# Performance work log

Hardware: AMD Instinct MI355X
Metric: run time of the kernel (lower is better)

Reference implementation:

```python
import jax, jax.numpy as jnp
import numpy as np

B, T, D = 4, 2048, 768
H = 12
HD = D // H
WINDOW = 128

def setup_inputs() -> dict:
    key = jax.random.key(0)
    k1, k2, k3 = jax.random.split(key, 3)
    x = jax.random.normal(k1, (B, T, D), dtype=jnp.float32)
    Wqkv = jax.random.normal(k2, (D, 3 * D), dtype=jnp.float32) * 0.02
    Wout = jax.random.normal(k3, (D, D), dtype=jnp.float32) * 0.02
    return {"x": x, "Wqkv": Wqkv, "Wout": Wout}

def reference(x, Wqkv, Wout):
    Bx, Tx, Dx = x.shape
    qkv = x @ Wqkv                      # [B,T,3D]
    q, k, v = jnp.split(qkv, 3, axis=-1)
    def heads(t):
        return t.reshape(Bx, Tx, H, HD).transpose(0, 2, 1, 3)  # [B,H,T,hd]
    q, k, v = heads(q), heads(k), heads(v)
    scale = 1.0 / jnp.sqrt(jnp.float32(HD))
    scores = jnp.einsum('bhqd,bhkd->bhqk', q, k) * scale       # [B,H,T,T]
    pos = jnp.arange(Tx)
    dist = pos[None, :] - pos[:, None]                          # j - i
    blocked = (dist > 0) | (dist < -WINDOW)                     # causal band
    scores = jnp.where(blocked[None, None], -jnp.inf, scores)
    attn = jax.nn.softmax(scores, axis=-1)
    out = jnp.einsum('bhqk,bhkd->bhqd', attn, v)                # [B,H,T,hd]
    out = out.transpose(0, 2, 1, 3).reshape(Bx, Tx, Dx)
    return out @ Wout
```

## Files before the change

### kernel.cpp

```cpp
#include <hip/hip_runtime.h>
#include <hip/hip_bf16.h>
#include <stdint.h>

typedef unsigned short u16;
typedef __attribute__((ext_vector_type(8))) short short8;
typedef __attribute__((ext_vector_type(8))) __bf16 bf16x8;
typedef __attribute__((ext_vector_type(4))) float f32x4;

constexpr int Bc  = 4;
constexpr int Tc  = 2048;
constexpr int Dc  = 768;
constexpr int Hc  = 12;
constexpr int WINc = 128;

static __device__ __forceinline__ u16 f2bf(float f) {
  union { float f; uint32_t u; } v; v.f = f;
  uint32_t u = v.u;
  return (u16)((u + 0x7fffu + ((u >> 16) & 1u)) >> 16);
}

static __device__ __forceinline__ f32x4 mfma16x16x32(bf16x8 a, bf16x8 b, f32x4 c) {
  return __builtin_amdgcn_mfma_f32_16x16x32_bf16(a, b, c, 0, 0, 0);
}

#define GLOAD_LDS16(gsrc, ldst)                                                \
  __builtin_amdgcn_global_load_lds(                                            \
      (const __attribute__((address_space(1))) void*)(gsrc),                   \
      (__attribute__((address_space(3))) void*)(ldst), 16, 0, 0)

__global__ __launch_bounds__(256) void prep(const float* __restrict__ x,
                                            u16* __restrict__ xb,
                                            const float* __restrict__ Wqkv,
                                            u16* __restrict__ wqkvT,
                                            const float* __restrict__ Wout,
                                            u16* __restrict__ woutT) {
  __shared__ float tile[64][65];
  const int t = threadIdx.x;
  const int b = blockIdx.x;
  if (b < 6144) {
    const int i = b * 256 + t;
    const float4 f = ((const float4*)x)[i];
    union { u16 h[4]; uint2 u; } pk;
    pk.h[0] = f2bf(f.x); pk.h[1] = f2bf(f.y); pk.h[2] = f2bf(f.z); pk.h[3] = f2bf(f.w);
    ((uint2*)xb)[i] = pk.u;
    return;
  }
  const float* W; u16* WT; int C, bx, by;
  if (b < 6576) { W = Wqkv; WT = wqkvT; C = 2304; const int bb = b - 6144; bx = bb % 36; by = bb / 36; }
  else          { W = Wout; WT = woutT; C = 768;  const int bb = b - 6576; bx = bb % 12; by = bb / 12; }
  const int R = 768;
  const int c0 = bx * 64, r0 = by * 64;
#pragma unroll
  for (int i = 0; i < 16; ++i) {
    const int e = i * 256 + t;
    const int r = e >> 6, c = e & 63;
    tile[r][c] = W[(size_t)(r0 + r) * C + c0 + c];
  }
  __syncthreads();
#pragma unroll
  for (int i = 0; i < 16; ++i) {
    const int e = i * 256 + t;
    const int r = e >> 6, c = e & 63;
    WT[(size_t)(c0 + r) * R + r0 + c] = f2bf(tile[c][r]);
  }
}

template <int EPI>
__global__ __launch_bounds__(256) void gemm_bt(const u16* __restrict__ A,
                                               const u16* __restrict__ Bt,
                                               u16* __restrict__ q_ws,
                                               u16* __restrict__ k_ws,
                                               u16* __restrict__ v_ws,
                                               float* __restrict__ fout) {
  __shared__ u16 As[2][128][64];
  __shared__ u16 Bs[2][128][64];
  const int t  = threadIdx.x;
  const int w  = t >> 6, l = t & 63;
  const int lr = l & 15, lh = l >> 4;
  const int wm = w >> 1, wn = w & 1;
  const int m0 = blockIdx.y * 128, n0 = blockIdx.x * 128;

  f32x4 acc[4][4];
#pragma unroll
  for (int mi = 0; mi < 4; ++mi)
#pragma unroll
    for (int ni = 0; ni < 4; ++ni) acc[mi][ni] = f32x4{0.f, 0.f, 0.f, 0.f};

  const int srow = w * 8 + (l >> 3);
  const int scol = ((l & 7) ^ (l >> 3)) * 8;
  const u16* aP = A  + (size_t)(m0 + srow) * 768 + scol;
  const u16* bP = Bt + (size_t)(n0 + srow) * 768 + scol;

#define STAGE(kt, b)                                                           \
  {                                                                            \
    const int ko_ = (kt) * 64;                                                 \
    char* asB_ = (char*)As + (b) * 16384 + w * 1024;                           \
    char* bsB_ = (char*)Bs + (b) * 16384 + w * 1024;                           \
    _Pragma("unroll")                                                          \
    for (int j = 0; j < 4; ++j) {                                              \
      GLOAD_LDS16(aP + ko_ + j * (32 * 768), asB_ + j * 4096);                 \
      GLOAD_LDS16(bP + ko_ + j * (32 * 768), bsB_ + j * 4096);                 \
    }                                                                          \
  }

#define COMPUTE(b)                                                             \
  {                                                                            \
    _Pragma("unroll")                                                          \
    for (int kk = 0; kk < 2; ++kk) {                                           \
      const int cb = (kk * 64 + lh * 16) ^ ((lr & 7) << 4);                    \
      bf16x8 af[4], bfr[4];                                                    \
      _Pragma("unroll")                                                        \
      for (int mi = 0; mi < 4; ++mi)                                           \
        af[mi] = *(const bf16x8*)((const char*)As + (b) * 16384 +              \
                                  (wm * 64 + mi * 16 + lr) * 128 + cb);        \
      _Pragma("unroll")                                                        \
      for (int ni = 0; ni < 4; ++ni)                                           \
        bfr[ni] = *(const bf16x8*)((const char*)Bs + (b) * 16384 +             \
                                   (wn * 64 + ni * 16 + lr) * 128 + cb);       \
      _Pragma("unroll")                                                        \
      for (int mi = 0; mi < 4; ++mi)                                           \
        _Pragma("unroll")                                                      \
        for (int ni = 0; ni < 4; ++ni)                                         \
          acc[mi][ni] = mfma16x16x32(af[mi], bfr[ni], acc[mi][ni]);            \
    }                                                                          \
  }

  STAGE(0, 0);
  for (int kt = 0; kt < 11; ++kt) {
    const int b = kt & 1;
    STAGE(kt + 1, b ^ 1);
    asm volatile("s_waitcnt vmcnt(8)" ::: "memory");
    __builtin_amdgcn_sched_barrier(0);
    __builtin_amdgcn_s_barrier();
    COMPUTE(b);
    __builtin_amdgcn_s_barrier();
  }
  asm volatile("s_waitcnt vmcnt(0)" ::: "memory");
  __builtin_amdgcn_sched_barrier(0);
  __builtin_amdgcn_s_barrier();
  COMPUTE(1);

#undef STAGE
#undef COMPUTE

  if (EPI == 0) {
#pragma unroll
    for (int mi = 0; mi < 4; ++mi)
#pragma unroll
      for (int ni = 0; ni < 4; ++ni) {
        const int col   = n0 + wn * 64 + ni * 16 + lr;
        const int which = col / 768;
        const int rem   = col - which * 768;
        const int h     = rem >> 6, d = rem & 63;
        u16* dst = (which == 0) ? q_ws : ((which == 1) ? k_ws : v_ws);
        const float scl = (which == 0) ? 0.125f : 1.0f;
#pragma unroll
        for (int r = 0; r < 4; ++r) {
          const int m  = m0 + wm * 64 + mi * 16 + lh * 4 + r;
          const int bb = m >> 11, tt = m & 2047;
          dst[(((size_t)(bb * Hc + h) * Tc + tt) << 6) + d] = f2bf(acc[mi][ni][r] * scl);
        }
      }
  } else {
#pragma unroll
    for (int mi = 0; mi < 4; ++mi)
#pragma unroll
      for (int ni = 0; ni < 4; ++ni) {
        const int col = n0 + wn * 64 + ni * 16 + lr;
#pragma unroll
        for (int r = 0; r < 4; ++r) {
          const int m = m0 + wm * 64 + mi * 16 + lh * 4 + r;
          fout[(size_t)m * 768 + col] = acc[mi][ni][r];
        }
      }
  }
}

__global__ __launch_bounds__(256) void swa_attn(const u16* __restrict__ Q,
                                                const u16* __restrict__ Kk,
                                                const u16* __restrict__ V,
                                                u16* __restrict__ Out) {
  __shared__ u16 Ks[3][64][72];
  __shared__ u16 Vt[3][64][72];
  __shared__ u16 Ps[2][4][16][72];

  const int t  = threadIdx.x;
  const int w  = t >> 6, l = t & 63;
  const int lr = l & 15, lh = l >> 4;
  const int bh = blockIdx.y;
  const int q0 = blockIdx.x * 64;
  const size_t hb = (size_t)bh * Tc * 64;

  const int kb_lo = (q0 >= WINc) ? q0 - WINc : 0;
  const int nt    = ((q0 - kb_lo) >> 6) + 1;

  const u16* qrow = Q + hb + (size_t)(q0 + w * 16 + lr) * 64;
  const bf16x8 qa0 = *(const bf16x8*)(qrow + lh * 8);
  const bf16x8 qa1 = *(const bf16x8*)(qrow + 32 + lh * 8);

  const int row = t >> 2, c = (t & 3) * 16;
  short8 kreg[3][2], vreg[3][2];
#pragma unroll
  for (int ti = 0; ti < 3; ++ti) {
    if (ti < nt) {
      const int kb = kb_lo + ti * 64;
      const short8* ksrc = (const short8*)(Kk + hb + (size_t)(kb + row) * 64 + c);
      const short8* vsrc = (const short8*)(V  + hb + (size_t)(kb + row) * 64 + c);
      kreg[ti][0] = ksrc[0]; kreg[ti][1] = ksrc[1];
      vreg[ti][0] = vsrc[0]; vreg[ti][1] = vsrc[1];
    }
  }
#pragma unroll
  for (int ti = 0; ti < 3; ++ti) {
    if (ti < nt) {
      *(short8*)&Ks[ti][row][c]     = kreg[ti][0];
      *(short8*)&Ks[ti][row][c + 8] = kreg[ti][1];
      const int rsw = row ^ c;
#pragma unroll
      for (int j = 0; j < 8; ++j) {
        Vt[ti][c + j][rsw]     = (u16)vreg[ti][0][j];
        Vt[ti][c + 8 + j][rsw] = (u16)vreg[ti][1][j];
      }
    }
  }
  __syncthreads();

  const short8 ones_i = {(short)0x3F80, (short)0x3F80, (short)0x3F80, (short)0x3F80,
                         (short)0x3F80, (short)0x3F80, (short)0x3F80, (short)0x3F80};
  const bf16x8 onesv = *(const bf16x8*)&ones_i;

  f32x4 s[3][4];
#pragma unroll
  for (int ti = 0; ti < 3; ++ti) {
    if (ti < nt) {
#pragma unroll
      for (int sub = 0; sub < 4; ++sub) {
        const bf16x8 kb0 = *(const bf16x8*)&Ks[ti][sub * 16 + lr][lh * 8];
        const bf16x8 kb1 = *(const bf16x8*)&Ks[ti][sub * 16 + lr][32 + lh * 8];
        f32x4 z = f32x4{0.f, 0.f, 0.f, 0.f};
        z = mfma16x16x32(qa0, kb0, z);
        z = mfma16x16x32(qa1, kb1, z);
        s[ti][sub] = z;
      }
    }
  }

  const int qbase = q0 + w * 16 + lh * 4;
#pragma unroll
  for (int ti = 0; ti < 3; ++ti) {
    if (ti < nt) {
      const int kb = kb_lo + ti * 64;
#pragma unroll
      for (int sub = 0; sub < 4; ++sub) {
        const int kj = kb + sub * 16 + lr;
#pragma unroll
        for (int r = 0; r < 4; ++r) {
          const int qi = qbase + r;
          const bool ok = (kj <= qi) && (kj + WINc >= qi);
          s[ti][sub][r] = ok ? s[ti][sub][r] : -1e30f;
        }
      }
    }
  }

  float m_r[4];
#pragma unroll
  for (int r = 0; r < 4; ++r) m_r[r] = -1e30f;
#pragma unroll
  for (int ti = 0; ti < 3; ++ti)
    if (ti < nt)
#pragma unroll
      for (int sub = 0; sub < 4; ++sub)
#pragma unroll
        for (int r = 0; r < 4; ++r)
          m_r[r] = fmaxf(m_r[r], s[ti][sub][r]);
#pragma unroll
  for (int msk = 1; msk < 16; msk <<= 1)
#pragma unroll
    for (int r = 0; r < 4; ++r)
      m_r[r] = fmaxf(m_r[r], __shfl_xor(m_r[r], msk, 64));

#pragma unroll
  for (int ti = 0; ti < 3; ++ti)
    if (ti < nt)
#pragma unroll
      for (int sub = 0; sub < 4; ++sub)
#pragma unroll
        for (int r = 0; r < 4; ++r)
          s[ti][sub][r] = __expf(s[ti][sub][r] - m_r[r]);

  f32x4 lacc = f32x4{0.f, 0.f, 0.f, 0.f};
  f32x4 Oa[4];
#pragma unroll
  for (int n = 0; n < 4; ++n) Oa[n] = f32x4{0.f, 0.f, 0.f, 0.f};

#pragma unroll
  for (int ti = 0; ti < 3; ++ti) {
    if (ti < nt) {
      const int pb = ti & 1;
#pragma unroll
      for (int sub = 0; sub < 4; ++sub)
#pragma unroll
        for (int r = 0; r < 4; ++r)
          Ps[pb][w][lh * 4 + r][sub * 16 + lr] = f2bf(s[ti][sub][r]);

#pragma unroll
      for (int ks = 0; ks < 2; ++ks) {
        const bf16x8 pa = *(const bf16x8*)&Ps[pb][w][lr][ks * 32 + lh * 8];
        lacc = mfma16x16x32(pa, onesv, lacc);
#pragma unroll
        for (int n = 0; n < 4; ++n) {
          const bf16x8 vb =
              *(const bf16x8*)&Vt[ti][n * 16 + lr][(ks * 32 + lh * 8) ^ (n * 16)];
          Oa[n] = mfma16x16x32(pa, vb, Oa[n]);
        }
      }
    }
  }

  const int bb = bh / Hc, h = bh - bb * Hc;
#pragma unroll
  for (int r = 0; r < 4; ++r) {
    const float inv = 1.f / lacc[r];
    const int ti_o = q0 + w * 16 + lh * 4 + r;
#pragma unroll
    for (int n = 0; n < 4; ++n)
      Out[((size_t)(bb * Tc + ti_o)) * 768 + h * 64 + n * 16 + lr] =
          f2bf(Oa[n][r] * inv);
  }
}

extern "C" void kernel_launch(void* const* d_in, const int* in_sizes, int n_in,
                              void* d_out, int out_size, void* d_ws, size_t ws_size,
                              hipStream_t stream) {
  (void)in_sizes; (void)n_in; (void)out_size; (void)ws_size;
  const float* x    = (const float*)d_in[0];
  const float* Wqkv = (const float*)d_in[1];
  const float* Wout = (const float*)d_in[2];
  float* out = (float*)d_out;

  u16* ws    = (u16*)d_ws;
  u16* xb    = ws;
  u16* wqkvT = xb + 6291456;
  u16* woutT = wqkvT + 1769472;
  u16* qws   = woutT + 589824;
  u16* kws   = qws + 6291456;
  u16* vws   = kws + 6291456;
  u16* aws   = xb;

  prep<<<6720, 256, 0, stream>>>(x, xb, Wqkv, wqkvT, Wout, woutT);
  gemm_bt<0><<<dim3(18, 64), 256, 0, stream>>>(xb, wqkvT, qws, kws, vws, nullptr);
  swa_attn<<<dim3(32, 48), 256, 0, stream>>>(qws, kws, vws, aws);
  gemm_bt<1><<<dim3(6, 64), 256, 0, stream>>>(aws, woutT, nullptr, nullptr, nullptr, out);
}
```

Baseline: 103.1 us.

## Fuse fp32-to-bf16 conversion of x into the QKV GEMM A-tile load

The separate prep pass that converted x to bf16 is removed. The QKV GEMM now reads fp32 x directly, converts it in registers and writes swizzled bf16 into LDS, which saves writing and re-reading a 12 MB bf16 copy of x. The new GEMM gives up the double-buffered async global-to-LDS pipeline for A and B, using a single buffer with syncthreads around it. It also reads A as fp32, so each A tile is fetched 18 times across the N blocks at twice the byte size, and load latency is exposed.

```diff
diff --git a/kernel.cpp b/kernel.cpp
--- a/kernel.cpp
+++ b/kernel.cpp
@@ -28,26 +28,16 @@
       (const __attribute__((address_space(1))) void*)(gsrc),                   \
       (__attribute__((address_space(3))) void*)(ldst), 16, 0, 0)
 
-__global__ __launch_bounds__(256) void prep(const float* __restrict__ x,
-                                            u16* __restrict__ xb,
-                                            const float* __restrict__ Wqkv,
+__global__ __launch_bounds__(256) void prep(const float* __restrict__ Wqkv,
                                             u16* __restrict__ wqkvT,
                                             const float* __restrict__ Wout,
                                             u16* __restrict__ woutT) {
   __shared__ float tile[64][65];
   const int t = threadIdx.x;
   const int b = blockIdx.x;
-  if (b < 6144) {
-    const int i = b * 256 + t;
-    const float4 f = ((const float4*)x)[i];
-    union { u16 h[4]; uint2 u; } pk;
-    pk.h[0] = f2bf(f.x); pk.h[1] = f2bf(f.y); pk.h[2] = f2bf(f.z); pk.h[3] = f2bf(f.w);
-    ((uint2*)xb)[i] = pk.u;
-    return;
-  }
   const float* W; u16* WT; int C, bx, by;
-  if (b < 6576) { W = Wqkv; WT = wqkvT; C = 2304; const int bb = b - 6144; bx = bb % 36; by = bb / 36; }
-  else          { W = Wout; WT = woutT; C = 768;  const int bb = b - 6576; bx = bb % 12; by = bb / 12; }
+  if (b < 432) { W = Wqkv; WT = wqkvT; C = 2304; bx = b % 36; by = b / 36; }
+  else         { W = Wout; WT = woutT; C = 768;  const int bb = b - 432; bx = bb % 12; by = bb / 12; }
   const int R = 768;
   const int c0 = bx * 64, r0 = by * 64;
 #pragma unroll
@@ -65,13 +55,91 @@
   }
 }
 
-template <int EPI>
-__global__ __launch_bounds__(256) void gemm_bt(const u16* __restrict__ A,
-                                               const u16* __restrict__ Bt,
-                                               u16* __restrict__ q_ws,
-                                               u16* __restrict__ k_ws,
-                                               u16* __restrict__ v_ws,
-                                               float* __restrict__ fout) {
+__global__ __launch_bounds__(256) void gemm_qkv(const float* __restrict__ A,
+                                                const u16* __restrict__ Bt,
+                                                u16* __restrict__ q_ws,
+                                                u16* __restrict__ k_ws,
+                                                u16* __restrict__ v_ws) {
+  __shared__ u16 As[128][64];
+  __shared__ u16 Bs[128][64];
+  const int t  = threadIdx.x;
+  const int w  = t >> 6, l = t & 63;
+  const int lr = l & 15, lh = l >> 4;
+  const int wm = w >> 1, wn = w & 1;
+  const int m0 = blockIdx.y * 128, n0 = blockIdx.x * 128;
+
+  f32x4 acc[4][4];
+#pragma unroll
+  for (int mi = 0; mi < 4; ++mi)
+#pragma unroll
+    for (int ni = 0; ni < 4; ++ni) acc[mi][ni] = f32x4{0.f, 0.f, 0.f, 0.f};
+
+  const int srow = w * 8 + (l >> 3);
+  const int scol = ((l & 7) ^ (l >> 3)) * 8;
+  const float* aP = A + (size_t)(m0 + srow) * 768 + scol;
+  const u16*   bP = Bt + (size_t)(n0 + srow) * 768 + scol;
+  char* asB = (char*)As + w * 1024;
+  char* bsB = (char*)Bs + w * 1024;
+
+  for (int kt = 0; kt < 12; ++kt) {
+    const int ko = kt * 64;
+    __syncthreads();
+#pragma unroll
+    for (int j = 0; j < 4; ++j)
+      GLOAD_LDS16(bP + ko + j * (32 * 768), bsB + j * 4096);
+#pragma unroll
+    for (int j = 0; j < 4; ++j) {
+      const float4 f0 = *(const float4*)(aP + ko + j * (32 * 768));
+      const float4 f1 = *(const float4*)(aP + ko + j * (32 * 768) + 4);
+      union { __hip_bfloat162 h2[4]; short8 s; } pk;
+      pk.h2[0] = __float22bfloat162_rn(float2{f0.x, f0.y});
+      pk.h2[1] = __float22bfloat162_rn(float2{f0.z, f0.w});
+      pk.h2[2] = __float22bfloat162_rn(float2{f1.x, f1.y});
+      pk.h2[3] = __float22bfloat162_rn(float2{f1.z, f1.w});
+      *(short8*)(asB + j * 4096 + l * 16) = pk.s;
+    }
+    __syncthreads();
+
+#pragma unroll
+    for (int kk = 0; kk < 2; ++kk) {
+      const int cb = (kk * 64 + lh * 16) ^ ((lr & 7) << 4);
+      bf16x8 af[4], bfr[4];
+#pragma unroll
+      for (int mi = 0; mi < 4; ++mi)
+        af[mi] = *(const bf16x8*)((const char*)As + (wm * 64 + mi * 16 + lr) * 128 + cb);
+#pragma unroll
+      for (int ni = 0; ni < 4; ++ni)
+        bfr[ni] = *(const bf16x8*)((const char*)Bs + (wn * 64 + ni * 16 + lr) * 128 + cb);
+#pragma unroll
+      for (int mi = 0; mi < 4; ++mi)
+#pragma unroll
+        for (int ni = 0; ni < 4; ++ni)
+          acc[mi][ni] = mfma16x16x32(af[mi], bfr[ni], acc[mi][ni]);
+    }
+  }
+
+#pragma unroll
+  for (int mi = 0; mi < 4; ++mi)
+#pragma unroll
+    for (int ni = 0; ni < 4; ++ni) {
+      const int col   = n0 + wn * 64 + ni * 16 + lr;
+      const int which = col / 768;
+      const int rem   = col - which * 768;
+      const int h     = rem >> 6, d = rem & 63;
+      u16* dst = (which == 0) ? q_ws : ((which == 1) ? k_ws : v_ws);
+      const float scl = (which == 0) ? 0.125f : 1.0f;
+#pragma unroll
+      for (int r = 0; r < 4; ++r) {
+        const int m  = m0 + wm * 64 + mi * 16 + lh * 4 + r;
+        const int bb = m >> 11, tt = m & 2047;
+        dst[(((size_t)(bb * Hc + h) * Tc + tt) << 6) + d] = f2bf(acc[mi][ni][r] * scl);
+      }
+    }
+}
+
+__global__ __launch_bounds__(256) void gemm_out(const u16* __restrict__ A,
+                                                const u16* __restrict__ Bt,
+                                                float* __restrict__ fout) {
   __shared__ u16 As[2][128][64];
   __shared__ u16 Bs[2][128][64];
   const int t  = threadIdx.x;
@@ -143,37 +211,17 @@
 #undef STAGE
 #undef COMPUTE
 
-  if (EPI == 0) {
-#pragma unroll
-    for (int mi = 0; mi < 4; ++mi)
-#pragma unroll
-      for (int ni = 0; ni < 4; ++ni) {
-        const int col   = n0 + wn * 64 + ni * 16 + lr;
-        const int which = col / 768;
-        const int rem   = col - which * 768;
-        const int h     = rem >> 6, d = rem & 63;
-        u16* dst = (which == 0) ? q_ws : ((which == 1) ? k_ws : v_ws);
-        const float scl = (which == 0) ? 0.125f : 1.0f;
-#pragma unroll
-        for (int r = 0; r < 4; ++r) {
-          const int m  = m0 + wm * 64 + mi * 16 + lh * 4 + r;
-          const int bb = m >> 11, tt = m & 2047;
-          dst[(((size_t)(bb * Hc + h) * Tc + tt) << 6) + d] = f2bf(acc[mi][ni][r] * scl);
-        }
-      }
-  } else {
-#pragma unroll
-    for (int mi = 0; mi < 4; ++mi)
-#pragma unroll
-      for (int ni = 0; ni < 4; ++ni) {
-        const int col = n0 + wn * 64 + ni * 16 + lr;
-#pragma unroll
-        for (int r = 0; r < 4; ++r) {
-          const int m = m0 + wm * 64 + mi * 16 + lh * 4 + r;
-          fout[(size_t)m * 768 + col] = acc[mi][ni][r];
-        }
-      }
-  }
+#pragma unroll
+  for (int mi = 0; mi < 4; ++mi)
+#pragma unroll
+    for (int ni = 0; ni < 4; ++ni) {
+      const int col = n0 + wn * 64 + ni * 16 + lr;
+#pragma unroll
+      for (int r = 0; r < 4; ++r) {
+        const int m = m0 + wm * 64 + mi * 16 + lh * 4 + r;
+        fout[(size_t)m * 768 + col] = acc[mi][ni][r];
+      }
+    }
 }
 
 __global__ __launch_bounds__(256) void swa_attn(const u16* __restrict__ Q,
@@ -340,16 +388,15 @@
   float* out = (float*)d_out;
 
   u16* ws    = (u16*)d_ws;
-  u16* xb    = ws;
-  u16* wqkvT = xb + 6291456;
+  u16* aws   = ws;
+  u16* wqkvT = aws + 6291456;
   u16* woutT = wqkvT + 1769472;
   u16* qws   = woutT + 589824;
   u16* kws   = qws + 6291456;
   u16* vws   = kws + 6291456;
-  u16* aws   = xb;
-
-  prep<<<6720, 256, 0, stream>>>(x, xb, Wqkv, wqkvT, Wout, woutT);
-  gemm_bt<0><<<dim3(18, 64), 256, 0, stream>>>(xb, wqkvT, qws, kws, vws, nullptr);
+
+  prep<<<576, 256, 0, stream>>>(Wqkv, wqkvT, Wout, woutT);
+  gemm_qkv<<<dim3(18, 64), 256, 0, stream>>>(x, wqkvT, qws, kws, vws);
   swa_attn<<<dim3(32, 48), 256, 0, stream>>>(qws, kws, vws, aws);
-  gemm_bt<1><<<dim3(6, 64), 256, 0, stream>>>(aws, woutT, nullptr, nullptr, nullptr, out);
-}
+  gemm_out<<<dim3(6, 64), 256, 0, stream>>>(aws, woutT, out);
+}
```

Result: slower. 108.1 us (+4.9%).
